# Performance work log

Hardware: AMD Instinct MI355X
Metric: run time of the kernel (lower is better)

## Reference

```python
import jax, jax.numpy as jnp
import numpy as np

D_MODEL = 2048
N_HEADS = 16
D_HEAD = D_MODEL // N_HEADS
SQLEN = 2048
EPS = 1e-5
XPOS_SCALE_BASE = 512.0


def apply_xpos(x, offset, inv=False):
    # x: (sqlen, d_head). Rotary embedding with xPos exponential length scaling.
    sqlen, d = x.shape
    half = d // 2
    freq = 1.0 / (10000.0 ** (jnp.arange(half, dtype=jnp.float32) / half))
    pos = jnp.arange(sqlen, dtype=jnp.float32) + offset  # absolute positions
    ang = pos[:, None] * freq[None, :]                   # (sqlen, half)
    sin, cos = jnp.sin(ang), jnp.cos(ang)
    # xPos per-dim scale zeta^(pos/scale_base); k gets the inverse scale.
    zeta = (jnp.arange(half, dtype=jnp.float32) * 2.0 + 0.4 * d) / (1.4 * d)
    sc = zeta[None, :] ** (pos[:, None] / XPOS_SCALE_BASE)
    if inv:
        sc = 1.0 / sc
    x1, x2 = x[:, :half], x[:, half:]
    r1 = (x1 * cos - x2 * sin) * sc
    r2 = (x2 * cos + x1 * sin) * sc
    return jnp.concatenate([r1, r2], axis=-1)


def group_norm(x, weight, bias):
    # x: (sqlen, d_model); n_heads groups of d_head channels each.
    xg = x.reshape(x.shape[0], N_HEADS, D_HEAD)
    mu = jnp.mean(xg, axis=-1, keepdims=True)
    var = jnp.mean((xg - mu) ** 2, axis=-1, keepdims=True)
    xn = ((xg - mu) * jax.lax.rsqrt(var + EPS)).reshape(x.shape)
    return xn * weight + bias


def setup_inputs() -> dict:
    key = jax.random.key(0)
    ks = jax.random.split(key, 9)
    s = 0.02
    return {
        "x": jax.random.normal(ks[0], (SQLEN, D_MODEL), dtype=jnp.float32),
        "state": jax.random.normal(ks[1], (N_HEADS, D_HEAD, D_HEAD), dtype=jnp.float32),
        "W_qkv": jax.random.normal(ks[2], (3 * D_MODEL, D_MODEL), dtype=jnp.float32) * s,
        "W_alpha": jax.random.normal(ks[3], (N_HEADS, D_MODEL), dtype=jnp.float32) * s,
        "b_alpha": jnp.zeros((N_HEADS,), dtype=jnp.float32),
        "alpha_base": jnp.log(jax.random.uniform(ks[4], (N_HEADS,), minval=0.95, maxval=0.999)).astype(jnp.float32),
        "gn_weight": jnp.ones((D_MODEL,), dtype=jnp.float32),
        "gn_bias": jnp.zeros((D_MODEL,), dtype=jnp.float32),
        "W_out": jax.random.normal(ks[5], (D_MODEL, D_MODEL), dtype=jnp.float32) * s,
        "W_gate": jax.random.normal(ks[6], (D_MODEL, D_MODEL), dtype=jnp.float32) * s,
        "offset": 0,
    }


def reference(x, state, W_qkv, W_alpha, b_alpha, alpha_base, gn_weight, gn_bias, W_out, W_gate, offset):
    sqlen = x.shape[0]
    # qkv projection -> (3, h, sqlen, d_head)
    qkv = (x @ W_qkv.T).reshape(sqlen, 3, N_HEADS, D_HEAD).transpose(1, 2, 0, 3)
    q, k, v = qkv[0], qkv[1], qkv[2]
    q = jax.vmap(lambda t: apply_xpos(t, offset))(q)
    k = jax.vmap(lambda t: apply_xpos(t, offset, inv=True))(k)

    # per-head, per-position decay log-rates: (h, sqlen), negative
    alphas = jax.nn.sigmoid(x @ W_alpha.T + b_alpha).T
    alphas = alpha_base[:, None] * 8.0 * alphas
    k = (1.0 - jnp.exp(alphas))[:, :, None] * k
    alphas = jnp.cumsum(alphas, axis=1)
    # causal decay matrix Delta[h,i,j] = exp(a_i - a_j) for j <= i
    Delta = jnp.tril(jnp.exp(alphas[:, :, None] - alphas[:, None, :]))

    attn = jnp.einsum('hid,hjd,hij->hij', q, k, Delta)
    ret = jnp.einsum('hij,hje->ihe', attn, v)  # (sqlen, h, d_head)

    # recurrent state carry
    new_state = jnp.exp(alphas[:, -1, None, None]) * state
    ret = ret + jnp.einsum('hid,hde,hi->ihe', q, state, jnp.exp(alphas))
    new_state = new_state + jnp.einsum('hid,hie,hi->hde', k, v, Delta[:, -1, :])

    ret = ret.reshape(sqlen, D_MODEL)
    ret = group_norm(ret, gn_weight, gn_bias)
    out = (jax.nn.swish(ret @ W_gate.T) * ret) @ W_out.T
    return (out, new_state)
```

## Files before the change

### kernel.cpp

```cpp
#include <hip/hip_runtime.h>
#include <cstddef>

#define SQLEN 2048
#define DMODEL 2048
#define NHEADS 16
#define DHEAD 128

typedef __attribute__((ext_vector_type(8))) short bf16x8;
typedef __attribute__((ext_vector_type(4))) float floatx4;

__device__ __forceinline__ unsigned short f2bf(float f) {
  union { float f; unsigned u; } c; c.f = f;
  unsigned u = c.u;
  unsigned r = u + 0x7fffu + ((u >> 16) & 1u);
  return (unsigned short)(r >> 16);
}
__device__ __forceinline__ float bf2f(unsigned short s) {
  union { unsigned u; float f; } c; c.u = ((unsigned)s) << 16;
  return c.f;
}

__global__ __launch_bounds__(256) void f2b_kernel(const float4* __restrict__ in,
                                                  ushort4* __restrict__ out) {
  int i = blockIdx.x * 256 + threadIdx.x;
  float4 v = in[i];
  ushort4 o;
  o.x = f2bf(v.x); o.y = f2bf(v.y); o.z = f2bf(v.z); o.w = f2bf(v.w);
  out[i] = o;
}

__global__ __launch_bounds__(256) void f2b2_kernel(const float4* __restrict__ in0,
                                                   ushort4* __restrict__ out0,
                                                   const float4* __restrict__ in1,
                                                   ushort4* __restrict__ out1,
                                                   int half_blocks) {
  int b = blockIdx.x;
  const float4* in = (b < half_blocks) ? in0 : in1;
  ushort4* out = (b < half_blocks) ? out0 : out1;
  int i = (b < half_blocks ? b : b - half_blocks) * 256 + threadIdx.x;
  float4 v = in[i];
  ushort4 o;
  o.x = f2bf(v.x); o.y = f2bf(v.y); o.z = f2bf(v.z); o.w = f2bf(v.w);
  out[i] = o;
}

#define GLD(srcp, dstp) __builtin_amdgcn_global_load_lds( \
    (const __attribute__((address_space(1))) unsigned int*)(srcp), \
    (__attribute__((address_space(3))) unsigned int*)(dstp), 16, 0, 0)

__global__ __launch_bounds__(512, 2) void gemm256_nt(const unsigned short* __restrict__ A,
                                                     const unsigned short* __restrict__ B,
                                                     float* __restrict__ C,
                                                     int M, int N, int K) {
  __shared__ __align__(16) unsigned short lds[65536];
  int tid = threadIdx.x;
  int wave = tid >> 6, lane = tid & 63;
  int wm = wave >> 2, wn = wave & 3;
  int quad = lane >> 4, m16 = lane & 15;
  int sw = m16 & 7;

  int nTN = gridDim.x;
  int lin = blockIdx.y * nTN + blockIdx.x;
  int nwg = gridDim.x * gridDim.y;
  int swzb = (nwg & 7) == 0 ? ((lin & 7) * (nwg >> 3) + (lin >> 3)) : lin;
  int row0 = (swzb / nTN) * 256, col0 = (swzb % nTN) * 256;

  const int nkt = K >> 6;
  const int nit = K >> 7;

  int srow = tid >> 3;
  int scol8 = (((tid & 7) ^ ((tid >> 3) & 7)) * 8);

  bf16x8 a0[2][4], a1[2][4], bb[2][2];
  floatx4 acc[2][2][4][2];
#pragma unroll
  for (int a = 0; a < 2; a++)
#pragma unroll
    for (int b = 0; b < 2; b++)
#pragma unroll
      for (int c = 0; c < 4; c++)
#pragma unroll
        for (int d = 0; d < 2; d++) acc[a][b][c][d] = (floatx4){0.f, 0.f, 0.f, 0.f};

#define STAGE(t_, ab_, h_) do { \
    int t2_ = (t_); if (t2_ >= nkt) t2_ -= nkt; \
    const unsigned short* gp_ = (ab_) ? B : A; \
    int rb_ = ((ab_) ? col0 : row0) + (h_) * 128 + srow; \
    int kk_ = t2_ * 64 + scol8; \
    unsigned bs_ = ((unsigned)((t_) & 1)) * 32768u + (ab_) * 16384u + (h_) * 8192u; \
    GLD(gp_ + (size_t)rb_ * K + kk_, lds + bs_ + tid * 8); \
    GLD(gp_ + (size_t)(rb_ + 64) * K + kk_, lds + bs_ + 4096 + tid * 8); \
  } while (0)

#define VMW asm volatile("s_waitcnt vmcnt(4)" ::: "memory");

#define RDA(dst_, BUF_, MH_) do { \
    const unsigned short* Ab_ = lds + (BUF_) * 32768 + (MH_) * 8192; \
    _Pragma("unroll") for (int ks = 0; ks < 2; ks++) \
      _Pragma("unroll") for (int fi = 0; fi < 4; fi++) \
        dst_[ks][fi] = *(const bf16x8*)(Ab_ + (wm * 64 + fi * 16 + m16) * 64 + (((ks * 4 + quad) ^ sw) * 8)); \
  } while (0)

#define RDB(BUF_, NH_) do { \
    const unsigned short* Bb_ = lds + (BUF_) * 32768 + 16384 + (NH_) * 8192; \
    _Pragma("unroll") for (int ks = 0; ks < 2; ks++) \
      _Pragma("unroll") for (int gj = 0; gj < 2; gj++) \
        bb[ks][gj] = *(const bf16x8*)(Bb_ + (wn * 32 + gj * 16 + m16) * 64 + (((ks * 4 + quad) ^ sw) * 8)); \
  } while (0)

#define MM(A_, MH_, NH_) \
    _Pragma("unroll") for (int ks = 0; ks < 2; ks++) \
      _Pragma("unroll") for (int fi = 0; fi < 4; fi++) \
        _Pragma("unroll") for (int gj = 0; gj < 2; gj++) \
          acc[MH_][NH_][fi][gj] = __builtin_amdgcn_mfma_f32_16x16x32_bf16( \
              A_[ks][fi], bb[ks][gj], acc[MH_][NH_][fi][gj], 0, 0, 0);

#define PH(RD_, STG_, W_, MM_) do { \
    RD_; \
    STG_; \
    W_ \
    __builtin_amdgcn_s_barrier(); \
    asm volatile("s_waitcnt lgkmcnt(0)" ::: "memory"); \
    __builtin_amdgcn_sched_barrier(0); \
    __builtin_amdgcn_s_setprio(1); \
    MM_ \
    __builtin_amdgcn_s_setprio(0); \
    __builtin_amdgcn_sched_barrier(0); \
    __builtin_amdgcn_s_barrier(); \
  } while (0)

  STAGE(0, 1, 0);
  STAGE(0, 0, 0);
  STAGE(0, 0, 1);
  STAGE(0, 1, 1);
  STAGE(1, 1, 0);
  STAGE(1, 0, 0);
  asm volatile("s_waitcnt vmcnt(4)" ::: "memory");
  __builtin_amdgcn_s_barrier();

  for (int it = 0; it < nit; ++it) {
    int T = it * 2;
    PH(RDA(a0, 0, 0); RDB(0, 0), STAGE(T + 1, 0, 1), , MM(a0, 0, 0));
    PH(RDA(a1, 0, 1),            STAGE(T + 1, 1, 1), , MM(a1, 1, 0));
    PH(RDB(0, 1),                STAGE(T + 2, 1, 0), , MM(a0, 0, 1));
    PH(,                         STAGE(T + 2, 0, 0), VMW, MM(a1, 1, 1));
    PH(RDA(a0, 1, 0); RDB(1, 0), STAGE(T + 2, 0, 1), , MM(a0, 0, 0));
    PH(RDA(a1, 1, 1),            STAGE(T + 2, 1, 1), , MM(a1, 1, 0));
    PH(RDB(1, 1),                STAGE(T + 3, 1, 0), , MM(a0, 0, 1));
    PH(,                         STAGE(T + 3, 0, 0), VMW, MM(a1, 1, 1));
  }

#pragma unroll
  for (int mh = 0; mh < 2; mh++)
#pragma unroll
    for (int nh = 0; nh < 2; nh++)
#pragma unroll
      for (int fi = 0; fi < 4; fi++)
#pragma unroll
        for (int gj = 0; gj < 2; gj++) {
          int rr = row0 + mh * 128 + wm * 64 + fi * 16 + quad * 4;
          int cc = col0 + nh * 128 + wn * 32 + gj * 16 + m16;
#pragma unroll
          for (int r = 0; r < 4; r++)
            C[(size_t)(rr + r) * N + cc] = acc[mh][nh][fi][gj][r];
        }
#undef PH
#undef MM
#undef RDB
#undef RDA
#undef VMW
#undef STAGE
}

__global__ __launch_bounds__(256) void gemm_bf16_nt(const unsigned short* __restrict__ A,
                                                    const unsigned short* __restrict__ B,
                                                    float* __restrict__ C,
                                                    int M, int N, int K) {
  __shared__ __align__(16) unsigned short As[128 * 32];
  __shared__ __align__(16) unsigned short Bs[128 * 32];
  int tid = threadIdx.x;
  int wave = tid >> 6;
  int lane = tid & 63;
  int wm = wave >> 1, wn = wave & 1;
  int quad = lane >> 4, m16 = lane & 15;
  int row0 = blockIdx.y * 128, col0 = blockIdx.x * 128;

  floatx4 acc[4][4];
#pragma unroll
  for (int i = 0; i < 4; i++)
#pragma unroll
    for (int j = 0; j < 4; j++) acc[i][j] = (floatx4){0.f, 0.f, 0.f, 0.f};

  int c0 = tid, c1 = tid + 256;
  int r0c = c0 >> 2, q0c = (c0 & 3) * 8;
  int r1c = c1 >> 2, q1c = (c1 & 3) * 8;

  const size_t sK = (size_t)K;
  for (int k0 = 0; k0 < K; k0 += 32) {
    __builtin_amdgcn_global_load_lds(
        (const __attribute__((address_space(1))) unsigned int*)(A + (size_t)(row0 + r0c) * sK + k0 + q0c),
        (__attribute__((address_space(3))) unsigned int*)(As + c0 * 8), 16, 0, 0);
    __builtin_amdgcn_global_load_lds(
        (const __attribute__((address_space(1))) unsigned int*)(A + (size_t)(row0 + r1c) * sK + k0 + q1c),
        (__attribute__((address_space(3))) unsigned int*)(As + c1 * 8), 16, 0, 0);
    __builtin_amdgcn_global_load_lds(
        (const __attribute__((address_space(1))) unsigned int*)(B + (size_t)(col0 + r0c) * sK + k0 + q0c),
        (__attribute__((address_space(3))) unsigned int*)(Bs + c0 * 8), 16, 0, 0);
    __builtin_amdgcn_global_load_lds(
        (const __attribute__((address_space(1))) unsigned int*)(B + (size_t)(col0 + r1c) * sK + k0 + q1c),
        (__attribute__((address_space(3))) unsigned int*)(Bs + c1 * 8), 16, 0, 0);
    __syncthreads();

    bf16x8 af[4], bfr[4];
#pragma unroll
    for (int i = 0; i < 4; i++)
      af[i] = *(const bf16x8*)(As + (wm * 64 + i * 16 + m16) * 32 + quad * 8);
#pragma unroll
    for (int j = 0; j < 4; j++)
      bfr[j] = *(const bf16x8*)(Bs + (wn * 64 + j * 16 + m16) * 32 + quad * 8);
#pragma unroll
    for (int i = 0; i < 4; i++)
#pragma unroll
      for (int j = 0; j < 4; j++)
        acc[i][j] = __builtin_amdgcn_mfma_f32_16x16x32_bf16(af[i], bfr[j], acc[i][j], 0, 0, 0);
    __syncthreads();
  }

#pragma unroll
  for (int i = 0; i < 4; i++) {
#pragma unroll
    for (int j = 0; j < 4; j++) {
      int rr = row0 + wm * 64 + i * 16 + quad * 4;
      int cc = col0 + wn * 64 + j * 16 + m16;
#pragma unroll
      for (int r = 0; r < 4; r++)
        C[(size_t)(rr + r) * N + cc] = acc[i][j][r];
    }
  }
}

__global__ __launch_bounds__(256) void gemm_swish_nt(const unsigned short* __restrict__ A,
                                                     const unsigned short* __restrict__ B,
                                                     const float* __restrict__ rn,
                                                     unsigned short* __restrict__ Hb,
                                                     int M, int N, int K) {
  __shared__ __align__(16) unsigned short As[128 * 32];
  __shared__ __align__(16) unsigned short Bs[128 * 32];
  int tid = threadIdx.x;
  int wave = tid >> 6;
  int lane = tid & 63;
  int wm = wave >> 1, wn = wave & 1;
  int quad = lane >> 4, m16 = lane & 15;
  int row0 = blockIdx.y * 128, col0 = blockIdx.x * 128;

  floatx4 acc[4][4];
#pragma unroll
  for (int i = 0; i < 4; i++)
#pragma unroll
    for (int j = 0; j < 4; j++) acc[i][j] = (floatx4){0.f, 0.f, 0.f, 0.f};

  int c0 = tid, c1 = tid + 256;
  int r0c = c0 >> 2, q0c = (c0 & 3) * 8;
  int r1c = c1 >> 2, q1c = (c1 & 3) * 8;

  const size_t sK = (size_t)K;
  for (int k0 = 0; k0 < K; k0 += 32) {
    __builtin_amdgcn_global_load_lds(
        (const __attribute__((address_space(1))) unsigned int*)(A + (size_t)(row0 + r0c) * sK + k0 + q0c),
        (__attribute__((address_space(3))) unsigned int*)(As + c0 * 8), 16, 0, 0);
    __builtin_amdgcn_global_load_lds(
        (const __attribute__((address_space(1))) unsigned int*)(A + (size_t)(row0 + r1c) * sK + k0 + q1c),
        (__attribute__((address_space(3))) unsigned int*)(As + c1 * 8), 16, 0, 0);
    __builtin_amdgcn_global_load_lds(
        (const __attribute__((address_space(1))) unsigned int*)(B + (size_t)(col0 + r0c) * sK + k0 + q0c),
        (__attribute__((address_space(3))) unsigned int*)(Bs + c0 * 8), 16, 0, 0);
    __builtin_amdgcn_global_load_lds(
        (const __attribute__((address_space(1))) unsigned int*)(B + (size_t)(col0 + r1c) * sK + k0 + q1c),
        (__attribute__((address_space(3))) unsigned int*)(Bs + c1 * 8), 16, 0, 0);
    __syncthreads();

    bf16x8 af[4], bfr[4];
#pragma unroll
    for (int i = 0; i < 4; i++)
      af[i] = *(const bf16x8*)(As + (wm * 64 + i * 16 + m16) * 32 + quad * 8);
#pragma unroll
    for (int j = 0; j < 4; j++)
      bfr[j] = *(const bf16x8*)(Bs + (wn * 64 + j * 16 + m16) * 32 + quad * 8);
#pragma unroll
    for (int i = 0; i < 4; i++)
#pragma unroll
      for (int j = 0; j < 4; j++)
        acc[i][j] = __builtin_amdgcn_mfma_f32_16x16x32_bf16(af[i], bfr[j], acc[i][j], 0, 0, 0);
    __syncthreads();
  }

#pragma unroll
  for (int i = 0; i < 4; i++) {
#pragma unroll
    for (int j = 0; j < 4; j++) {
      int rr = row0 + wm * 64 + i * 16 + quad * 4;
      int cc = col0 + wn * 64 + j * 16 + m16;
#pragma unroll
      for (int r = 0; r < 4; r++) {
        float g = acc[i][j][r];
        float rv = rn[(size_t)(rr + r) * N + cc];
        float hh = g / (1.f + __expf(-g)) * rv;
        Hb[(size_t)(rr + r) * N + cc] = f2bf(hh);
      }
    }
  }
}

__global__ __launch_bounds__(256) void alpha_kernel(const float* __restrict__ x,
                                                    const float* __restrict__ W_alpha,
                                                    const float* __restrict__ b_alpha,
                                                    const float* __restrict__ alpha_base,
                                                    float* __restrict__ a_raw) {
  __shared__ float xs[4][2048];
  int tid = threadIdx.x;
  int t0 = blockIdx.x * 4;
#pragma unroll
  for (int p = 0; p < 8; p++) {
    int idx = tid + p * 256;
    int row = idx >> 9, c4 = idx & 511;
    *(float4*)&xs[row][c4 * 4] = *(const float4*)(x + (size_t)(t0 + row) * DMODEL + c4 * 4);
  }
  __syncthreads();
  int w = tid >> 6, lane = tid & 63;
  int t = t0 + w;
#pragma unroll
  for (int h = 0; h < NHEADS; h++) {
    const float4* wr = (const float4*)(W_alpha + (size_t)h * DMODEL);
    float s = 0.f;
#pragma unroll
    for (int i = lane; i < 512; i += 64) {
      float4 a = *(const float4*)&xs[w][i * 4];
      float4 b = wr[i];
      s += a.x * b.x + a.y * b.y + a.z * b.z + a.w * b.w;
    }
#pragma unroll
    for (int off = 32; off > 0; off >>= 1) s += __shfl_down(s, off);
    if (lane == 0) {
      float sig = 1.f / (1.f + __expf(-(s + b_alpha[h])));
      a_raw[(size_t)h * SQLEN + t] = alpha_base[h] * 8.f * sig;
    }
  }
}

__global__ __launch_bounds__(256) void cumsum_kernel(const float* __restrict__ a_raw,
                                                     float* __restrict__ A) {
  int h = blockIdx.x;
  __shared__ float part[256];
  int tid = threadIdx.x;
  float v[8];
  float s = 0.f;
#pragma unroll
  for (int i = 0; i < 8; i++) {
    v[i] = a_raw[(size_t)h * SQLEN + tid * 8 + i];
    s += v[i];
  }
  part[tid] = s;
  __syncthreads();
  for (int off = 1; off < 256; off <<= 1) {
    float tmp = (tid >= off) ? part[tid - off] : 0.f;
    __syncthreads();
    part[tid] += tmp;
    __syncthreads();
  }
  float run = (tid > 0) ? part[tid - 1] : 0.f;
#pragma unroll
  for (int i = 0; i < 8; i++) {
    run += v[i];
    A[(size_t)h * SQLEN + tid * 8 + i] = run;
  }
}

__global__ __launch_bounds__(256) void xpos_kernel(const float* __restrict__ qkv,
                                                   const float* __restrict__ a_raw,
                                                   const int* __restrict__ offset_p,
                                                   unsigned short* __restrict__ qb,
                                                   unsigned short* __restrict__ kb,
                                                   unsigned short* __restrict__ vb) {
  int idx = blockIdx.x * 256 + threadIdx.x;
  int j = idx & 63;
  int t = (idx >> 6) & 2047;
  int h = idx >> 17;
  float pos = (float)(t + offset_p[0]);
  float freq = exp2f(-(float)j * (13.287712379549449f / 64.f));
  float ang = pos * freq;
  float sn = __sinf(ang), cs = __cosf(ang);
  float zeta = (2.f * (float)j + 51.2f) / 179.2f;
  float lzp = __log2f(zeta) * pos * (1.f / 512.f);
  float sc = exp2f(lzp);
  float sci = exp2f(-lzp);
  const float* row = qkv + (size_t)t * (3 * DMODEL);
  int base = h * DHEAD + j;
  float q1 = row[base], q2 = row[base + 64];
  float k1 = row[DMODEL + base], k2 = row[DMODEL + base + 64];
  float v1 = row[2 * DMODEL + base], v2 = row[2 * DMODEL + base + 64];
  size_t o = ((size_t)h * SQLEN + t) * DHEAD + j;
  qb[o] = f2bf((q1 * cs - q2 * sn) * sc);
  qb[o + 64] = f2bf((q2 * cs + q1 * sn) * sc);
  float km = (1.f - __expf(a_raw[(size_t)h * SQLEN + t])) * sci;
  kb[o] = f2bf((k1 * cs - k2 * sn) * km);
  kb[o + 64] = f2bf((k2 * cs + k1 * sn) * km);
  vb[o] = f2bf(v1);
  vb[o + 64] = f2bf(v2);
}

__global__ __launch_bounds__(256) void transpose_kv_kernel(const unsigned short* __restrict__ kb,
                                                           const unsigned short* __restrict__ vb,
                                                           const float* __restrict__ A,
                                                           unsigned short* __restrict__ kT,
                                                           unsigned short* __restrict__ vT) {
  __shared__ __align__(16) unsigned short tile[64][72];
  int h = blockIdx.z >> 1, sel = blockIdx.z & 1;
  int t0 = blockIdx.x * 64, d0 = blockIdx.y * 64;
  int tid = threadIdx.x;
  const unsigned short* src = (sel ? vb : kb) + ((size_t)h * SQLEN + t0) * DHEAD + d0;
  unsigned short* dst = (sel ? vT : kT) + (size_t)h * (DHEAD * SQLEN) + (size_t)d0 * SQLEN + t0;
  float B = A[(size_t)h * SQLEN + SQLEN - 1];
#pragma unroll
  for (int p = 0; p < 2; p++) {
    int c = tid + p * 256;
    int r = c >> 3, off = (c & 7) * 8;
    bf16x8 in = *(const bf16x8*)(src + (size_t)r * DHEAD + off);
    if (!sel) {
      float w = __expf(B - A[(size_t)h * SQLEN + t0 + r]);
      bf16x8 o;
#pragma unroll
      for (int j = 0; j < 8; j++) o[j] = (short)f2bf(bf2f((unsigned short)in[j]) * w);
      *(bf16x8*)&tile[r][off] = o;
    } else {
      *(bf16x8*)&tile[r][off] = in;
    }
  }
  __syncthreads();
#pragma unroll
  for (int p = 0; p < 2; p++) {
    int c = tid + p * 256;
    int dr = c >> 3, toff = (c & 7) * 8;
    bf16x8 o;
#pragma unroll
    for (int j = 0; j < 8; j++) o[j] = (short)tile[toff + j][dr];
    *(bf16x8*)(dst + (size_t)dr * SQLEN + toff) = o;
  }
}

__global__ __launch_bounds__(256) void transpose_state_kernel(const float* __restrict__ st,
                                                              unsigned short* __restrict__ stT) {
  __shared__ float tile[64][65];
  int h = blockIdx.z, d0 = blockIdx.x * 64, e0 = blockIdx.y * 64;
  int tid = threadIdx.x;
  const float* src = st + (size_t)h * 16384 + (size_t)d0 * DHEAD + e0;
#pragma unroll
  for (int p = 0; p < 4; p++) {
    int idx = tid + p * 256;
    int r = idx >> 4, c = (idx & 15) * 4;
    float4 f = *(const float4*)(src + (size_t)r * DHEAD + c);
    tile[r][c] = f.x; tile[r][c + 1] = f.y; tile[r][c + 2] = f.z; tile[r][c + 3] = f.w;
  }
  __syncthreads();
  unsigned short* dst = stT + (size_t)h * 16384 + (size_t)e0 * DHEAD + d0;
#pragma unroll
  for (int p = 0; p < 2; p++) {
    int idx = tid + p * 256;
    int er = idx >> 3, doff = (idx & 7) * 8;
    bf16x8 o;
#pragma unroll
    for (int j = 0; j < 8; j++) o[j] = (short)f2bf(tile[doff + j][er]);
    *(bf16x8*)(dst + (size_t)er * DHEAD + doff) = o;
  }
}

__global__ __launch_bounds__(256) void retention_mfma(const unsigned short* __restrict__ qb,
                                                      const unsigned short* __restrict__ kb,
                                                      const unsigned short* __restrict__ vT,
                                                      const unsigned short* __restrict__ stT,
                                                      const float* __restrict__ A,
                                                      const float* __restrict__ gn_w,
                                                      const float* __restrict__ gn_b,
                                                      float* __restrict__ rn,
                                                      unsigned short* __restrict__ rnb) {
  __shared__ __align__(16) unsigned short ks[2][64 * 128];
  __shared__ __align__(16) unsigned short vs[2][128 * 64];
  __shared__ __align__(16) unsigned short Ss[64 * 72];
  int h = blockIdx.x;
  int i0 = blockIdx.y * 64;
  int tid = threadIdx.x;
  int wave = tid >> 6, lane = tid & 63, quad = lane >> 4, m16 = lane & 15;
  const float* Ah = A + (size_t)h * SQLEN;
  float c = Ah[i0];
  int rq = wave * 16 + m16;

  const unsigned short* qh = qb + ((size_t)h * SQLEN + i0 + rq) * DHEAD;
  bf16x8 qf[4];
#pragma unroll
  for (int dc = 0; dc < 4; dc++)
    qf[dc] = *(const bf16x8*)(qh + dc * 32 + quad * 8);
  float ei = __expf(Ah[i0 + rq] - c);

  float wg[8], bg[8];
#pragma unroll
  for (int et = 0; et < 8; et++) {
    int col = h * DHEAD + et * 16 + m16;
    wg[et] = gn_w[col];
    bg[et] = gn_b[col];
  }

  bool skipl = false;
  if (lane < 32) {
    int j0l = lane * 64;
    if (j0l <= i0) skipl = (c - Ah[j0l + 63] < -87.f);
  }
  unsigned long long smask = __ballot(skipl);
  int j_start = 64 * (int)__builtin_ctzll(~smask);

  floatx4 acc[8];
#pragma unroll
  for (int et = 0; et < 8; et++) acc[et] = (floatx4){0.f, 0.f, 0.f, 0.f};

  const unsigned short* khb = kb + (size_t)h * SQLEN * DHEAD;
  const unsigned short* vhb = vT + (size_t)h * (DHEAD * SQLEN);

#define STAGE_KV(b_, j0_) do { \
    const unsigned short* kh_ = khb + (size_t)(j0_) * DHEAD; \
    const unsigned short* vh_ = vhb + (j0_); \
    _Pragma("unroll") for (int p = 0; p < 4; p++) { \
      int cch = tid + p * 256; \
      int r_ = cch >> 4, kp_ = (cch & 15) ^ (r_ & 7); \
      GLD(kh_ + (size_t)r_ * DHEAD + kp_ * 8, &ks[b_][0] + cch * 8); \
      int e_ = cch >> 3, tp_ = (cch & 7) ^ (e_ & 7); \
      GLD(vh_ + (size_t)e_ * SQLEN + tp_ * 8, &vs[b_][0] + cch * 8); \
    } \
  } while (0)

  STAGE_KV(0, j_start);

  if (c > -87.f) {
    const unsigned short* sp = stT + (size_t)h * 16384;
    float ecr[4];
#pragma unroll
    for (int r = 0; r < 4; r++) ecr[r] = __expf(Ah[i0 + wave * 16 + quad * 4 + r]);
#pragma unroll
    for (int et = 0; et < 8; et++) {
#pragma unroll
      for (int dc = 0; dc < 4; dc++) {
        bf16x8 sf = *(const bf16x8*)(sp + (et * 16 + m16) * DHEAD + dc * 32 + quad * 8);
        acc[et] = __builtin_amdgcn_mfma_f32_16x16x32_bf16(qf[dc], sf, acc[et], 0, 0, 0);
      }
#pragma unroll
      for (int r = 0; r < 4; r++) acc[et][r] *= ecr[r];
    }
  }

  int cur = 0;
  for (int j0 = j_start; j0 <= i0; j0 += 64) {
    int nxt = j0 + 64;
    float av = Ah[j0 + lane];
    __builtin_amdgcn_sched_barrier(0);
    if (nxt <= i0) {
      STAGE_KV(cur ^ 1, nxt);
      asm volatile("s_waitcnt vmcnt(8) lgkmcnt(0)" ::: "memory");
    } else {
      asm volatile("s_waitcnt vmcnt(0) lgkmcnt(0)" ::: "memory");
    }
    __builtin_amdgcn_sched_barrier(0);
    asm volatile("s_barrier" ::: "memory");

    float dj = __expf(c - av);

    bool diag = (j0 == i0);
    const unsigned short* ksc = &ks[cur][0];
    const unsigned short* vsc = &vs[cur][0];
#pragma unroll
    for (int jt = 0; jt < 4; jt++) {
      floatx4 s = (floatx4){0.f, 0.f, 0.f, 0.f};
#pragma unroll
      for (int dc = 0; dc < 4; dc++) {
        int rk = jt * 16 + m16;
        bf16x8 kf = *(const bf16x8*)(ksc + rk * 128 + (((dc * 4 + quad) ^ (rk & 7)) * 8));
        s = __builtin_amdgcn_mfma_f32_16x16x32_bf16(kf, qf[dc], s, 0, 0, 0);
      }
      int jb = jt * 16 + quad * 4;
      float d0 = __shfl(dj, jb + 0);
      float d1 = __shfl(dj, jb + 1);
      float d2 = __shfl(dj, jb + 2);
      float d3 = __shfl(dj, jb + 3);
      ushort4 pk;
      pk.x = f2bf((diag && (jb + 0 > rq)) ? 0.f : s[0] * ei * d0);
      pk.y = f2bf((diag && (jb + 1 > rq)) ? 0.f : s[1] * ei * d1);
      pk.z = f2bf((diag && (jb + 2 > rq)) ? 0.f : s[2] * ei * d2);
      pk.w = f2bf((diag && (jb + 3 > rq)) ? 0.f : s[3] * ei * d3);
      *(ushort4*)(Ss + rq * 72 + jb) = pk;
    }

    bf16x8 sfr[2];
#pragma unroll
    for (int kc = 0; kc < 2; kc++)
      sfr[kc] = *(const bf16x8*)(Ss + rq * 72 + kc * 32 + quad * 8);
#pragma unroll
    for (int et = 0; et < 8; et++) {
#pragma unroll
      for (int kc = 0; kc < 2; kc++) {
        int e = et * 16 + m16;
        bf16x8 vf = *(const bf16x8*)(vsc + e * 64 + (((kc * 4 + quad) ^ (e & 7)) * 8));
        acc[et] = __builtin_amdgcn_mfma_f32_16x16x32_bf16(sfr[kc], vf, acc[et], 0, 0, 0);
      }
    }
    asm volatile("s_barrier" ::: "memory");
    cur ^= 1;
  }
#undef STAGE_KV

#pragma unroll
  for (int r = 0; r < 4; r++) {
    float s = 0.f, ss = 0.f;
#pragma unroll
    for (int et = 0; et < 8; et++) {
      float v = acc[et][r];
      s += v; ss += v * v;
    }
#pragma unroll
    for (int off = 8; off > 0; off >>= 1) {
      s += __shfl_xor(s, off);
      ss += __shfl_xor(ss, off);
    }
    float mu = s * (1.f / 128.f);
    float var = ss * (1.f / 128.f) - mu * mu;
    float inv = rsqrtf(var + 1e-5f);
    int row = i0 + wave * 16 + quad * 4 + r;
    size_t o = (size_t)row * DMODEL + h * DHEAD;
#pragma unroll
    for (int et = 0; et < 8; et++) {
      float rv = (acc[et][r] - mu) * inv * wg[et] + bg[et];
      rn[o + et * 16 + m16] = rv;
      rnb[o + et * 16 + m16] = f2bf(rv);
    }
  }
}

__global__ __launch_bounds__(256) void state_gemm(const unsigned short* __restrict__ kT,
                                                  const unsigned short* __restrict__ vT,
                                                  float* __restrict__ P) {
  __shared__ __align__(16) unsigned short As[128 * 32];
  __shared__ __align__(16) unsigned short Bs[128 * 32];
  int chunk = blockIdx.x, h = blockIdx.y;
  int tid = threadIdx.x;
  int wave = tid >> 6, lane = tid & 63;
  int wm = wave >> 1, wn = wave & 1;
  int quad = lane >> 4, m16 = lane & 15;
  const unsigned short* Ab = kT + (size_t)h * (DHEAD * SQLEN);
  const unsigned short* Bb = vT + (size_t)h * (DHEAD * SQLEN);

  floatx4 acc[4][4];
#pragma unroll
  for (int i = 0; i < 4; i++)
#pragma unroll
    for (int j = 0; j < 4; j++) acc[i][j] = (floatx4){0.f, 0.f, 0.f, 0.f};

  int c0 = tid, c1 = tid + 256;
  int r0c = c0 >> 2, q0c = (c0 & 3) * 8;
  int r1c = c1 >> 2, q1c = (c1 & 3) * 8;

  for (int k0 = chunk * 256; k0 < chunk * 256 + 256; k0 += 32) {
    __builtin_amdgcn_global_load_lds(
        (const __attribute__((address_space(1))) unsigned int*)(Ab + (size_t)r0c * SQLEN + k0 + q0c),
        (__attribute__((address_space(3))) unsigned int*)(As + c0 * 8), 16, 0, 0);
    __builtin_amdgcn_global_load_lds(
        (const __attribute__((address_space(1))) unsigned int*)(Ab + (size_t)r1c * SQLEN + k0 + q1c),
        (__attribute__((address_space(3))) unsigned int*)(As + c1 * 8), 16, 0, 0);
    __builtin_amdgcn_global_load_lds(
        (const __attribute__((address_space(1))) unsigned int*)(Bb + (size_t)r0c * SQLEN + k0 + q0c),
        (__attribute__((address_space(3))) unsigned int*)(Bs + c0 * 8), 16, 0, 0);
    __builtin_amdgcn_global_load_lds(
        (const __attribute__((address_space(1))) unsigned int*)(Bb + (size_t)r1c * SQLEN + k0 + q1c),
        (__attribute__((address_space(3))) unsigned int*)(Bs + c1 * 8), 16, 0, 0);
    __syncthreads();

    bf16x8 af[4], bfr[4];
#pragma unroll
    for (int i = 0; i < 4; i++)
      af[i] = *(const bf16x8*)(As + (wm * 64 + i * 16 + m16) * 32 + quad * 8);
#pragma unroll
    for (int j = 0; j < 4; j++)
      bfr[j] = *(const bf16x8*)(Bs + (wn * 64 + j * 16 + m16) * 32 + quad * 8);
#pragma unroll
    for (int i = 0; i < 4; i++)
#pragma unroll
      for (int j = 0; j < 4; j++)
        acc[i][j] = __builtin_amdgcn_mfma_f32_16x16x32_bf16(af[i], bfr[j], acc[i][j], 0, 0, 0);
    __syncthreads();
  }

  float* Pp = P + (size_t)(h * 8 + chunk) * 16384;
#pragma unroll
  for (int i = 0; i < 4; i++)
#pragma unroll
    for (int j = 0; j < 4; j++) {
      int rr = wm * 64 + i * 16 + quad * 4;
      int cc = wn * 64 + j * 16 + m16;
#pragma unroll
      for (int r = 0; r < 4; r++)
        Pp[(size_t)(rr + r) * DHEAD + cc] = acc[i][j][r];
    }
}

__global__ __launch_bounds__(256) void state_combine(const float* __restrict__ P,
                                                     const float* __restrict__ state,
                                                     const float* __restrict__ A,
                                                     float* __restrict__ out_state) {
  int idx = blockIdx.x * 256 + threadIdx.x;
  int h = idx >> 14;
  int de = idx & 16383;
  float B = A[(size_t)h * SQLEN + SQLEN - 1];
  float s = __expf(B) * state[idx];
#pragma unroll
  for (int c = 0; c < 8; c++) s += P[(size_t)(h * 8 + c) * 16384 + de];
  out_state[idx] = s;
}

extern "C" void kernel_launch(void* const* d_in, const int* in_sizes, int n_in,
                              void* d_out, int out_size, void* d_ws, size_t ws_size,
                              hipStream_t stream) {
  const float* x = (const float*)d_in[0];
  const float* state = (const float*)d_in[1];
  const float* W_qkv = (const float*)d_in[2];
  const float* W_alpha = (const float*)d_in[3];
  const float* b_alpha = (const float*)d_in[4];
  const float* alpha_base = (const float*)d_in[5];
  const float* gn_w = (const float*)d_in[6];
  const float* gn_b = (const float*)d_in[7];
  const float* W_out = (const float*)d_in[8];
  const float* W_gate = (const float*)d_in[9];
  const int* offset = (const int*)d_in[10];

  float* ws = (float*)d_ws;
  float* qkv = ws;
  float* P   = ws + 4194304;
  float* rn  = ws + 29360128;
  float* araw = ws + 33554432;
  float* Acum = ws + 33587200;

  unsigned short* xb    = (unsigned short*)(ws + 12582912);
  unsigned short* Wqkvb = (unsigned short*)(ws + 16777216);
  unsigned short* qb    = (unsigned short*)(ws + 12582912);
  unsigned short* kb    = (unsigned short*)(ws + 14680064);
  unsigned short* vb    = (unsigned short*)(ws + 16777216);
  unsigned short* kT_s  = (unsigned short*)(ws + 18874368);
  unsigned short* vT_b  = (unsigned short*)(ws + 20971520);
  unsigned short* stT_b = (unsigned short*)(ws + 23068672);
  unsigned short* rnb   = (unsigned short*)(ws + 25165824);
  unsigned short* Wgateb = (unsigned short*)(ws + 14680064);
  unsigned short* Woutb  = (unsigned short*)(ws + 16777216);
  unsigned short* Hb     = (unsigned short*)(ws + 18874368);

  float* out = (float*)d_out;
  float* out_state = out + 4194304;

  dim3 blk(256);
  f2b2_kernel<<<dim3(16384), blk, 0, stream>>>((const float4*)x, (ushort4*)xb,
                                               (const float4*)W_qkv, (ushort4*)Wqkvb, 4096);
  gemm256_nt<<<dim3(24, 8), dim3(512), 0, stream>>>(xb, Wqkvb, qkv, 2048, 6144, 2048);

  alpha_kernel<<<dim3(512), blk, 0, stream>>>(x, W_alpha, b_alpha, alpha_base, araw);
  cumsum_kernel<<<dim3(16), blk, 0, stream>>>(araw, Acum);
  xpos_kernel<<<dim3(8192), blk, 0, stream>>>(qkv, araw, offset, qb, kb, vb);
  transpose_kv_kernel<<<dim3(32, 2, 32), blk, 0, stream>>>(kb, vb, Acum, kT_s, vT_b);
  transpose_state_kernel<<<dim3(2, 2, 16), blk, 0, stream>>>(state, stT_b);

  retention_mfma<<<dim3(16, 32), blk, 0, stream>>>(qb, kb, vT_b, stT_b, Acum,
                                                   gn_w, gn_b, rn, rnb);
  state_gemm<<<dim3(8, 16), blk, 0, stream>>>(kT_s, vT_b, P);
  state_combine<<<dim3(1024), blk, 0, stream>>>(P, state, Acum, out_state);

  f2b2_kernel<<<dim3(8192), blk, 0, stream>>>((const float4*)W_gate, (ushort4*)Wgateb,
                                              (const float4*)W_out, (ushort4*)Woutb, 4096);
  gemm_swish_nt<<<dim3(16, 16), blk, 0, stream>>>(rnb, Wgateb, rn, Hb, 2048, 2048, 2048);
  gemm_bf16_nt<<<dim3(16, 16), blk, 0, stream>>>(Hb, Woutb, out, 2048, 2048, 2048);
}
```

Before: 418.5 us.

## Split retention over key chunks with atomic accumulation and separate group-norm pass

The retention kernel gains a third grid dimension that splits the causal key range into 512-wide chunks. Each block accumulates its partial output into a zeroed fp32 buffer with atomicAdd, and a new kernel then applies the group norm and writes the fp32 and bf16 outputs. This is meant to fix load imbalance and low occupancy when 512 blocks do triangular work of very uneven length. In exchange it adds a zero pass, atomic traffic, an extra full read and write of the result, and order-dependent floating-point sums.

Result: slower. 429.9 us (+2.7%).

```diff
diff --git a/kernel.cpp b/kernel.cpp
--- a/kernel.cpp
+++ b/kernel.cpp
@@ -42,6 +42,10 @@
   ushort4 o;
   o.x = f2bf(v.x); o.y = f2bf(v.y); o.z = f2bf(v.z); o.w = f2bf(v.w);
   out[i] = o;
+}
+
+__global__ __launch_bounds__(256) void zero_kernel(float4* __restrict__ p) {
+  p[blockIdx.x * 256 + threadIdx.x] = (float4){0.f, 0.f, 0.f, 0.f};
 }
 
 #define GLD(srcp, dstp) __builtin_amdgcn_global_load_lds( \
@@ -473,41 +477,27 @@
   }
 }
 
-__global__ __launch_bounds__(256) void retention_mfma(const unsigned short* __restrict__ qb,
-                                                      const unsigned short* __restrict__ kb,
-                                                      const unsigned short* __restrict__ vT,
-                                                      const unsigned short* __restrict__ stT,
-                                                      const float* __restrict__ A,
-                                                      const float* __restrict__ gn_w,
-                                                      const float* __restrict__ gn_b,
-                                                      float* __restrict__ rn,
-                                                      unsigned short* __restrict__ rnb) {
+__global__ __launch_bounds__(256) void retention_partial(const unsigned short* __restrict__ qb,
+                                                         const unsigned short* __restrict__ kb,
+                                                         const unsigned short* __restrict__ vT,
+                                                         const unsigned short* __restrict__ stT,
+                                                         const float* __restrict__ A,
+                                                         float* __restrict__ R32) {
   __shared__ __align__(16) unsigned short ks[2][64 * 128];
   __shared__ __align__(16) unsigned short vs[2][128 * 64];
   __shared__ __align__(16) unsigned short Ss[64 * 72];
   int h = blockIdx.x;
   int i0 = blockIdx.y * 64;
+  int jc = blockIdx.z;
+  int jlo = jc * 512;
+  if (jlo > i0) return;
+  int jhi = min(i0, jlo + 448);
   int tid = threadIdx.x;
   int wave = tid >> 6, lane = tid & 63, quad = lane >> 4, m16 = lane & 15;
   const float* Ah = A + (size_t)h * SQLEN;
   float c = Ah[i0];
   int rq = wave * 16 + m16;
 
-  const unsigned short* qh = qb + ((size_t)h * SQLEN + i0 + rq) * DHEAD;
-  bf16x8 qf[4];
-#pragma unroll
-  for (int dc = 0; dc < 4; dc++)
-    qf[dc] = *(const bf16x8*)(qh + dc * 32 + quad * 8);
-  float ei = __expf(Ah[i0 + rq] - c);
-
-  float wg[8], bg[8];
-#pragma unroll
-  for (int et = 0; et < 8; et++) {
-    int col = h * DHEAD + et * 16 + m16;
-    wg[et] = gn_w[col];
-    bg[et] = gn_b[col];
-  }
-
   bool skipl = false;
   if (lane < 32) {
     int j0l = lane * 64;
@@ -515,6 +505,17 @@
   }
   unsigned long long smask = __ballot(skipl);
   int j_start = 64 * (int)__builtin_ctzll(~smask);
+  int j_begin = max(j_start, jlo);
+  bool work = (j_begin <= jhi);
+  bool crossw = (jc == 0) && (c > -87.f);
+  if (!work && !crossw) return;
+
+  const unsigned short* qh = qb + ((size_t)h * SQLEN + i0 + rq) * DHEAD;
+  bf16x8 qf[4];
+#pragma unroll
+  for (int dc = 0; dc < 4; dc++)
+    qf[dc] = *(const bf16x8*)(qh + dc * 32 + quad * 8);
+  float ei = __expf(Ah[i0 + rq] - c);
 
   floatx4 acc[8];
 #pragma unroll
@@ -535,9 +536,9 @@
     } \
   } while (0)
 
-  STAGE_KV(0, j_start);
-
-  if (c > -87.f) {
+  if (work) STAGE_KV(0, j_begin);
+
+  if (crossw) {
     const unsigned short* sp = stT + (size_t)h * 16384;
     float ecr[4];
 #pragma unroll
@@ -554,90 +555,114 @@
     }
   }
 
-  int cur = 0;
-  for (int j0 = j_start; j0 <= i0; j0 += 64) {
-    int nxt = j0 + 64;
-    float av = Ah[j0 + lane];
-    __builtin_amdgcn_sched_barrier(0);
-    if (nxt <= i0) {
-      STAGE_KV(cur ^ 1, nxt);
-      asm volatile("s_waitcnt vmcnt(8) lgkmcnt(0)" ::: "memory");
-    } else {
-      asm volatile("s_waitcnt vmcnt(0) lgkmcnt(0)" ::: "memory");
+  if (work) {
+    int cur = 0;
+    for (int j0 = j_begin; j0 <= jhi; j0 += 64) {
+      int nxt = j0 + 64;
+      float av = Ah[j0 + lane];
+      __builtin_amdgcn_sched_barrier(0);
+      if (nxt <= jhi) {
+        STAGE_KV(cur ^ 1, nxt);
+        asm volatile("s_waitcnt vmcnt(8) lgkmcnt(0)" ::: "memory");
+      } else {
+        asm volatile("s_waitcnt vmcnt(0) lgkmcnt(0)" ::: "memory");
+      }
+      __builtin_amdgcn_sched_barrier(0);
+      asm volatile("s_barrier" ::: "memory");
+
+      float dj = __expf(c - av);
+
+      bool diag = (j0 == i0);
+      const unsigned short* ksc = &ks[cur][0];
+      const unsigned short* vsc = &vs[cur][0];
+#pragma unroll
+      for (int jt = 0; jt < 4; jt++) {
+        floatx4 s = (floatx4){0.f, 0.f, 0.f, 0.f};
+#pragma unroll
+        for (int dc = 0; dc < 4; dc++) {
+          int rk = jt * 16 + m16;
+          bf16x8 kf = *(const bf16x8*)(ksc + rk * 128 + (((dc * 4 + quad) ^ (rk & 7)) * 8));
+          s = __builtin_amdgcn_mfma_f32_16x16x32_bf16(kf, qf[dc], s, 0, 0, 0);
+        }
+        int jb = jt * 16 + quad * 4;
+        float d0 = __shfl(dj, jb + 0);
+        float d1 = __shfl(dj, jb + 1);
+        float d2 = __shfl(dj, jb + 2);
+        float d3 = __shfl(dj, jb + 3);
+        ushort4 pk;
+        pk.x = f2bf((diag && (jb + 0 > rq)) ? 0.f : s[0] * ei * d0);
+        pk.y = f2bf((diag && (jb + 1 > rq)) ? 0.f : s[1] * ei * d1);
+        pk.z = f2bf((diag && (jb + 2 > rq)) ? 0.f : s[2] * ei * d2);
+        pk.w = f2bf((diag && (jb + 3 > rq)) ? 0.f : s[3] * ei * d3);
+        *(ushort4*)(Ss + rq * 72 + jb) = pk;
+      }
+
+      bf16x8 sfr[2];
+#pragma unroll
+      for (int kc = 0; kc < 2; kc++)
+        sfr[kc] = *(const bf16x8*)(Ss + rq * 72 + kc * 32 + quad * 8);
+#pragma unroll
+      for (int et = 0; et < 8; et++) {
+#pragma unroll
+        for (int kc = 0; kc < 2; kc++) {
+          int e = et * 16 + m16;
+          bf16x8 vf = *(const bf16x8*)(vsc + e * 64 + (((kc * 4 + quad) ^ (e & 7)) * 8));
+          acc[et] = __builtin_amdgcn_mfma_f32_16x16x32_bf16(sfr[kc], vf, acc[et], 0, 0, 0);
+        }
+      }
+      asm volatile("s_barrier" ::: "memory");
+      cur ^= 1;
     }
-    __builtin_amdgcn_sched_barrier(0);
-    asm volatile("s_barrier" ::: "memory");
-
-    float dj = __expf(c - av);
-
-    bool diag = (j0 == i0);
-    const unsigned short* ksc = &ks[cur][0];
-    const unsigned short* vsc = &vs[cur][0];
-#pragma unroll
-    for (int jt = 0; jt < 4; jt++) {
-      floatx4 s = (floatx4){0.f, 0.f, 0.f, 0.f};
-#pragma unroll
-      for (int dc = 0; dc < 4; dc++) {
-        int rk = jt * 16 + m16;
-        bf16x8 kf = *(const bf16x8*)(ksc + rk * 128 + (((dc * 4 + quad) ^ (rk & 7)) * 8));
-        s = __builtin_amdgcn_mfma_f32_16x16x32_bf16(kf, qf[dc], s, 0, 0, 0);
-      }
-      int jb = jt * 16 + quad * 4;
-      float d0 = __shfl(dj, jb + 0);
-      float d1 = __shfl(dj, jb + 1);
-      float d2 = __shfl(dj, jb + 2);
-      float d3 = __shfl(dj, jb + 3);
-      ushort4 pk;
-      pk.x = f2bf((diag && (jb + 0 > rq)) ? 0.f : s[0] * ei * d0);
-      pk.y = f2bf((diag && (jb + 1 > rq)) ? 0.f : s[1] * ei * d1);
-      pk.z = f2bf((diag && (jb + 2 > rq)) ? 0.f : s[2] * ei * d2);
-      pk.w = f2bf((diag && (jb + 3 > rq)) ? 0.f : s[3] * ei * d3);
-      *(ushort4*)(Ss + rq * 72 + jb) = pk;
-    }
-
-    bf16x8 sfr[2];
-#pragma unroll
-    for (int kc = 0; kc < 2; kc++)
-      sfr[kc] = *(const bf16x8*)(Ss + rq * 72 + kc * 32 + quad * 8);
-#pragma unroll
-    for (int et = 0; et < 8; et++) {
-#pragma unroll
-      for (int kc = 0; kc < 2; kc++) {
-        int e = et * 16 + m16;
-        bf16x8 vf = *(const bf16x8*)(vsc + e * 64 + (((kc * 4 + quad) ^ (e & 7)) * 8));
-        acc[et] = __builtin_amdgcn_mfma_f32_16x16x32_bf16(sfr[kc], vf, acc[et], 0, 0, 0);
-      }
-    }
-    asm volatile("s_barrier" ::: "memory");
-    cur ^= 1;
   }
 #undef STAGE_KV
 
 #pragma unroll
   for (int r = 0; r < 4; r++) {
-    float s = 0.f, ss = 0.f;
-#pragma unroll
-    for (int et = 0; et < 8; et++) {
-      float v = acc[et][r];
-      s += v; ss += v * v;
-    }
-#pragma unroll
-    for (int off = 8; off > 0; off >>= 1) {
-      s += __shfl_xor(s, off);
-      ss += __shfl_xor(ss, off);
-    }
-    float mu = s * (1.f / 128.f);
-    float var = ss * (1.f / 128.f) - mu * mu;
-    float inv = rsqrtf(var + 1e-5f);
     int row = i0 + wave * 16 + quad * 4 + r;
     size_t o = (size_t)row * DMODEL + h * DHEAD;
 #pragma unroll
-    for (int et = 0; et < 8; et++) {
-      float rv = (acc[et][r] - mu) * inv * wg[et] + bg[et];
-      rn[o + et * 16 + m16] = rv;
-      rnb[o + et * 16 + m16] = f2bf(rv);
-    }
-  }
+    for (int et = 0; et < 8; et++)
+      atomicAdd(&R32[o + et * 16 + m16], acc[et][r]);
+  }
+}
+
+__global__ __launch_bounds__(256) void gn_kernel(const float* __restrict__ R32,
+                                                 const float* __restrict__ gn_w,
+                                                 const float* __restrict__ gn_b,
+                                                 float* __restrict__ rn,
+                                                 unsigned short* __restrict__ rnb) {
+  int row = blockIdx.x;
+  int tid = threadIdx.x;
+  const float* src = R32 + (size_t)row * DMODEL + tid * 8;
+  float4 a = *(const float4*)src;
+  float4 b = *(const float4*)(src + 4);
+  float s = a.x + a.y + a.z + a.w + b.x + b.y + b.z + b.w;
+  float ss = a.x * a.x + a.y * a.y + a.z * a.z + a.w * a.w +
+             b.x * b.x + b.y * b.y + b.z * b.z + b.w * b.w;
+#pragma unroll
+  for (int off = 8; off > 0; off >>= 1) {
+    s += __shfl_xor(s, off);
+    ss += __shfl_xor(ss, off);
+  }
+  float mu = s * (1.f / 128.f);
+  float var = ss * (1.f / 128.f) - mu * mu;
+  float inv = rsqrtf(var + 1e-5f);
+  int col0 = tid * 8;
+  const float* wp = gn_w + col0;
+  const float* bp = gn_b + col0;
+  float v[8] = {a.x, a.y, a.z, a.w, b.x, b.y, b.z, b.w};
+  float o[8];
+  ushort4 ob[2];
+#pragma unroll
+  for (int k = 0; k < 8; k++) {
+    o[k] = (v[k] - mu) * inv * wp[k] + bp[k];
+    ((unsigned short*)ob)[k] = f2bf(o[k]);
+  }
+  float* rp = rn + (size_t)row * DMODEL + col0;
+  *(float4*)rp = (float4){o[0], o[1], o[2], o[3]};
+  *(float4*)(rp + 4) = (float4){o[4], o[5], o[6], o[7]};
+  *(ushort4*)(rnb + (size_t)row * DMODEL + col0) = ob[0];
+  *(ushort4*)(rnb + (size_t)row * DMODEL + col0 + 4) = ob[1];
 }
 
 __global__ __launch_bounds__(256) void state_gemm(const unsigned short* __restrict__ kT,
@@ -737,7 +762,8 @@
 
   float* ws = (float*)d_ws;
   float* qkv = ws;
-  float* P   = ws + 4194304;
+  float* R32 = ws + 4194304;
+  float* P   = ws + 8388608;
   float* rn  = ws + 29360128;
   float* araw = ws + 33554432;
   float* Acum = ws + 33587200;
@@ -766,11 +792,13 @@
   alpha_kernel<<<dim3(512), blk, 0, stream>>>(x, W_alpha, b_alpha, alpha_base, araw);
   cumsum_kernel<<<dim3(16), blk, 0, stream>>>(araw, Acum);
   xpos_kernel<<<dim3(8192), blk, 0, stream>>>(qkv, araw, offset, qb, kb, vb);
+  zero_kernel<<<dim3(4096), blk, 0, stream>>>((float4*)R32);
   transpose_kv_kernel<<<dim3(32, 2, 32), blk, 0, stream>>>(kb, vb, Acum, kT_s, vT_b);
   transpose_state_kernel<<<dim3(2, 2, 16), blk, 0, stream>>>(state, stT_b);
 
-  retention_mfma<<<dim3(16, 32), blk, 0, stream>>>(qb, kb, vT_b, stT_b, Acum,
-                                                   gn_w, gn_b, rn, rnb);
+  retention_partial<<<dim3(16, 32, 4), blk, 0, stream>>>(qb, kb, vT_b, stT_b, Acum, R32);
+  gn_kernel<<<dim3(2048), blk, 0, stream>>>(R32, gn_w, gn_b, rn, rnb);
+
   state_gemm<<<dim3(8, 16), blk, 0, stream>>>(kT_s, vT_b, P);
   state_combine<<<dim3(1024), blk, 0, stream>>>(P, state, Acum, out_state);
 
```
